# Optimization experiments

Measured on AMD Instinct MI355X. Metric: run time of the kernel, lower is better.

## Reference

```python
import jax, jax.numpy as jnp
import numpy as np

N_HEADS = 16

def setup_inputs() -> dict:
    key = jax.random.key(0)
    ks = jax.random.split(key, 4)
    B, T, C = 4, 2048, 1024
    x = jax.random.normal(ks[0], (B, T, C), dtype=jnp.float32)
    w_qkv = jax.random.normal(ks[1], (C, 3 * C), dtype=jnp.float32) * (1.0 / np.sqrt(C))
    b_qkv = jnp.zeros((3 * C,), dtype=jnp.float32)
    w_proj = jax.random.normal(ks[2], (C, C), dtype=jnp.float32) * (1.0 / np.sqrt(C))
    b_proj = jnp.zeros((C,), dtype=jnp.float32)
    return {"x": x, "w_qkv": w_qkv, "b_qkv": b_qkv, "w_proj": w_proj, "b_proj": b_proj}

def reference(x, w_qkv, b_qkv, w_proj, b_proj):
    B, T, C = x.shape
    H = N_HEADS
    d = C // H
    qkv = x @ w_qkv + b_qkv                       # [B,T,3C]
    q, k, v = jnp.split(qkv, 3, axis=-1)
    # [B,T,C] -> [B,H,T,d]
    q = q.reshape(B, T, H, d).transpose(0, 2, 1, 3)
    k = k.reshape(B, T, H, d).transpose(0, 2, 1, 3)
    v = v.reshape(B, T, H, d).transpose(0, 2, 1, 3)
    scale = 1.0 / np.sqrt(d).astype(np.float32)
    logits = jnp.einsum('bhqd,bhkd->bhqk', q, k) * scale  # [B,H,T,T]
    causal = jnp.tril(jnp.ones((T, T), dtype=bool))
    logits = jnp.where(causal, logits, jnp.finfo(logits.dtype).min)
    attn = jax.nn.softmax(logits, axis=-1)
    out = jnp.einsum('bhqk,bhkd->bhqd', attn, v)          # [B,H,T,d]
    out = out.transpose(0, 2, 1, 3).reshape(B, T, C)
    return out @ w_proj + b_proj
```

## Files before the change

### kernel.cpp

```cpp
#include <hip/hip_runtime.h>
#include <hip/hip_bf16.h>


typedef unsigned short u16;
typedef __bf16 bf16_t;
typedef bf16_t bf16x8 __attribute__((ext_vector_type(8)));
typedef float f32x4 __attribute__((ext_vector_type(4)));
typedef u16 u16x8 __attribute__((ext_vector_type(8)));
typedef const __attribute__((address_space(1))) void* as1cv;
typedef __attribute__((address_space(3))) void* as3v;

#define BB 4
#define TT 2048
#define CC 1024
#define HH 16
#define DD 64

static __device__ __forceinline__ u16 f2bf(float f) {
  union { float f; unsigned int u; } x; x.f = f;
  unsigned int u = x.u;
  u += 0x7fff + ((u >> 16) & 1);
  return (u16)(u >> 16);
}

static __device__ __forceinline__ unsigned int pack2(float lo, float hi) {
  return __builtin_amdgcn_perm(__float_as_uint(hi), __float_as_uint(lo),
                               0x07060302u);
}

__global__ __launch_bounds__(256) void cast_f32_bf16(
    const float* __restrict__ in, u16* __restrict__ out) {
  int i = (blockIdx.x * 256 + threadIdx.x) * 4;
  float4 v = *(const float4*)(in + i);
  ushort4 o;
  o.x = f2bf(v.x); o.y = f2bf(v.y); o.z = f2bf(v.z); o.w = f2bf(v.w);
  *(ushort4*)(out + i) = o;
}

__global__ __launch_bounds__(256) void transpose_cast(
    const float* __restrict__ in, u16* __restrict__ out, int K, int N) {
  __shared__ float tile[32][33];
  int n0 = blockIdx.x * 32, k0 = blockIdx.y * 32;
  int tx = threadIdx.x & 31, ty = threadIdx.x >> 5;
#pragma unroll
  for (int i = 0; i < 32; i += 8)
    tile[ty + i][tx] = in[(size_t)(k0 + ty + i) * N + n0 + tx];
  __syncthreads();
#pragma unroll
  for (int i = 0; i < 32; i += 8)
    out[(size_t)(n0 + ty + i) * K + k0 + tx] = f2bf(tile[tx][ty + i]);
}

__global__ __launch_bounds__(256) void gemm_bt(
    const u16* __restrict__ A, const u16* __restrict__ Bt,
    const float* __restrict__ bias,
    int M, int N, int K, int mode,
    u16* __restrict__ qb, u16* __restrict__ kb, u16* __restrict__ vt,
    float* __restrict__ outf) {
  __shared__ u16 As[128][64];
  __shared__ u16 Bs[128][64];
  const int tid = threadIdx.x;
  const int lane = tid & 63, wave = tid >> 6;
  const int quad = lane >> 4, l16 = lane & 15;
  const int wy = wave >> 1, wx = wave & 1;
  const int m0 = blockIdx.x * 128, n0 = blockIdx.y * 128;
  const int srow = lane >> 3, sblk = (lane & 7) ^ (lane >> 3);
  const int rsw = l16 & 7;

  f32x4 acc[4][4] = {};

  for (int k0 = 0; k0 < K; k0 += 64) {
#pragma unroll
    for (int i = 0; i < 4; i++) {
      int lr = wave * 32 + i * 8;
      int row = lr + srow;
      __builtin_amdgcn_global_load_lds(
          (as1cv)(A + (size_t)(m0 + row) * K + k0 + sblk * 8),
          (as3v)(&As[lr][0]), 16, 0, 0);
      __builtin_amdgcn_global_load_lds(
          (as1cv)(Bt + (size_t)(n0 + row) * K + k0 + sblk * 8),
          (as3v)(&Bs[lr][0]), 16, 0, 0);
    }
    __syncthreads();
#pragma unroll
    for (int ks = 0; ks < 2; ks++) {
      const int pcol = ((ks * 4 + quad) ^ rsw) * 8;
      bf16x8 af[4], bfr[4];
#pragma unroll
      for (int i = 0; i < 4; i++)
        af[i] = *(const bf16x8*)&As[wy * 64 + i * 16 + l16][pcol];
#pragma unroll
      for (int j = 0; j < 4; j++)
        bfr[j] = *(const bf16x8*)&Bs[wx * 64 + j * 16 + l16][pcol];
#pragma unroll
      for (int i = 0; i < 4; i++)
#pragma unroll
        for (int j = 0; j < 4; j++)
          acc[i][j] = __builtin_amdgcn_mfma_f32_16x16x32_bf16(af[i], bfr[j], acc[i][j], 0, 0, 0);
    }
    __syncthreads();
  }

  if (mode == 1) {
#pragma unroll
    for (int i = 0; i < 4; i++)
#pragma unroll
      for (int j = 0; j < 4; j++) {
        int nn = n0 + wx * 64 + j * 16 + l16;
        float bv = bias[nn];
#pragma unroll
        for (int r = 0; r < 4; r++) {
          int mm = m0 + wy * 64 + i * 16 + quad * 4 + r;
          outf[(size_t)mm * N + nn] = acc[i][j][r] + bv;
        }
      }
  } else {
    const int b = m0 >> 11;
    const int tb = (m0 & 2047) + wy * 64 + quad * 4;
    if (n0 < 1024) {
#pragma unroll
      for (int j = 0; j < 4; j++) {
        int nn = n0 + wx * 64 + j * 16 + l16;
        int h = nn >> 6, dd = nn & 63;
        float bv = bias[nn];
        u16* base = qb + ((size_t)(b * HH + h) * TT) * DD + dd;
#pragma unroll
        for (int i = 0; i < 4; i++)
#pragma unroll
          for (int r = 0; r < 4; r++)
            base[(size_t)(tb + i * 16 + r) * DD] =
                f2bf((acc[i][j][r] + bv) * 0.1803368801111f);
      }
    } else if (n0 < 2048) {
#pragma unroll
      for (int j = 0; j < 4; j++) {
        int nn = n0 + wx * 64 + j * 16 + l16;
        int rem = nn & 1023, h = rem >> 6, dd = rem & 63;
        float bv = bias[nn];
        u16* base = kb + ((size_t)(b * HH + h) * TT) * DD + dd;
#pragma unroll
        for (int i = 0; i < 4; i++)
#pragma unroll
          for (int r = 0; r < 4; r++)
            base[(size_t)(tb + i * 16 + r) * DD] = f2bf(acc[i][j][r] + bv);
      }
    } else {
#pragma unroll
      for (int j = 0; j < 4; j++) {
        int nn = n0 + wx * 64 + j * 16 + l16;
        int rem = nn & 1023, h = rem >> 6, dd = rem & 63;
        float bv = bias[nn];
        u16* base = vt + ((size_t)(b * HH + h) * DD + dd) * TT;
#pragma unroll
        for (int i = 0; i < 4; i++)
#pragma unroll
          for (int r = 0; r < 4; r++)
            base[tb + i * 16 + r] = f2bf(acc[i][j][r] + bv);
      }
    }
  }
}

__global__ __launch_bounds__(256, 3) void attn_kernel(
    const u16* __restrict__ q_buf, const u16* __restrict__ k_buf,
    const u16* __restrict__ v_t, u16* __restrict__ attn_out) {
  __shared__ __align__(16) u16 Ks[64][64];
  __shared__ __align__(16) u16 Vs[64][64];
  __shared__ __align__(16) u16 Pl[4][16][64];
  const int tid = threadIdx.x;
  const int lane = tid & 63, wave = tid >> 6;
  const int quad = lane >> 4, l16 = lane & 15;
  const int bh = blockIdx.x;
  const int b = bh >> 4, h = bh & 15;
  const int tile = 15 - (int)blockIdx.y;
  const int qt0 = tile * 128;
  const int qw = qt0 + wave * 32;
  const u16* Q = q_buf + (size_t)bh * TT * DD;
  const u16* Kp = k_buf + (size_t)bh * TT * DD;
  const u16* Vt = v_t + (size_t)bh * DD * TT;

  const int srow = lane >> 3;
  const int sblk = (lane & 7) ^ srow;
  const int swz = l16 & 7;

  bf16x8 qf[2][2];
#pragma unroll
  for (int f = 0; f < 2; f++)
#pragma unroll
    for (int h2 = 0; h2 < 2; h2++)
      qf[f][h2] = *(const bf16x8*)(Q + (size_t)(qw + f * 16 + l16) * DD + h2 * 32 + quad * 8);

  f32x4 o[2][4] = {};
  float l_p[2] = {0.f, 0.f};

  const int my_end = qw + 32;
  const int kv_stop = qt0 + 128;
  for (int kv0 = 0; kv0 < kv_stop; kv0 += 64) {
#pragma unroll
    for (int i = 0; i < 2; i++) {
      int r = wave * 16 + i * 8 + srow;
      __builtin_amdgcn_global_load_lds(
          (as1cv)(Kp + (size_t)(kv0 + r) * DD + sblk * 8),
          (as3v)(&Ks[wave * 16 + i * 8][0]), 16, 0, 0);
      __builtin_amdgcn_global_load_lds(
          (as1cv)(Vt + (size_t)r * TT + kv0 + sblk * 8),
          (as3v)(&Vs[wave * 16 + i * 8][0]), 16, 0, 0);
    }
    __syncthreads();

    if (kv0 < my_end) {
      const bool edge = (kv0 + 63 > qw);
      f32x4 s[2][4] = {};
#pragma unroll
      for (int kg = 0; kg < 4; kg++) {
        bf16x8 ka = *(const bf16x8*)&Ks[kg * 16 + l16][(quad ^ swz) * 8];
        bf16x8 kb2 = *(const bf16x8*)&Ks[kg * 16 + l16][((4 + quad) ^ swz) * 8];
#pragma unroll
        for (int f = 0; f < 2; f++) {
          s[f][kg] = __builtin_amdgcn_mfma_f32_16x16x32_bf16(ka, qf[f][0], s[f][kg], 0, 0, 0);
          s[f][kg] = __builtin_amdgcn_mfma_f32_16x16x32_bf16(kb2, qf[f][1], s[f][kg], 0, 0, 0);
        }
      }
#pragma unroll
      for (int f = 0; f < 2; f++) {
        const int qi = qw + f * 16 + l16;
#pragma unroll
        for (int kg = 0; kg < 4; kg++) {
          float v0 = s[f][kg][0], v1 = s[f][kg][1], v2 = s[f][kg][2], v3 = s[f][kg][3];
          if (edge) {
            int kvb = kv0 + kg * 16 + quad * 4;
            v0 = (kvb + 0 <= qi) ? v0 : -1e30f;
            v1 = (kvb + 1 <= qi) ? v1 : -1e30f;
            v2 = (kvb + 2 <= qi) ? v2 : -1e30f;
            v3 = (kvb + 3 <= qi) ? v3 : -1e30f;
          }
          float e0 = __builtin_amdgcn_exp2f(v0);
          float e1 = __builtin_amdgcn_exp2f(v1);
          float e2 = __builtin_amdgcn_exp2f(v2);
          float e3 = __builtin_amdgcn_exp2f(v3);
          l_p[f] += (e0 + e1) + (e2 + e3);
          uint2 pk;
          pk.x = pack2(e0, e1);
          pk.y = pack2(e2, e3);
          *(uint2*)&Pl[wave][l16][((kg * 2 + (quad >> 1)) ^ swz) * 8 + (quad & 1) * 4] = pk;
        }
        __threadfence_block();
#pragma unroll
        for (int c = 0; c < 2; c++) {
          bf16x8 pa = *(const bf16x8*)&Pl[wave][l16][((c * 4 + quad) ^ swz) * 8];
#pragma unroll
          for (int g = 0; g < 4; g++) {
            bf16x8 vr = *(const bf16x8*)&Vs[g * 16 + l16][((c * 4 + quad) ^ swz) * 8];
            o[f][g] = __builtin_amdgcn_mfma_f32_16x16x32_bf16(vr, pa, o[f][g], 0, 0, 0);
          }
        }
      }
    }
    __syncthreads();
  }

#pragma unroll
  for (int f = 0; f < 2; f++) {
    float l = l_p[f];
    l += __shfl_xor(l, 16);
    l += __shfl_xor(l, 32);
    float inv_l = 1.0f / l;
    int trow = qw + f * 16 + l16;
#pragma unroll
    for (int g = 0; g < 4; g++) {
      ushort4 st;
      st.x = f2bf(o[f][g][0] * inv_l);
      st.y = f2bf(o[f][g][1] * inv_l);
      st.z = f2bf(o[f][g][2] * inv_l);
      st.w = f2bf(o[f][g][3] * inv_l);
      *(ushort4*)(attn_out + ((size_t)(b * TT + trow)) * CC + h * DD + g * 16 + quad * 4) = st;
    }
  }
}

extern "C" void kernel_launch(void* const* d_in, const int* in_sizes, int n_in,
                              void* d_out, int out_size, void* d_ws, size_t ws_size,
                              hipStream_t stream) {
  const float* x = (const float*)d_in[0];
  const float* w_qkv = (const float*)d_in[1];
  const float* b_qkv = (const float*)d_in[2];
  const float* w_proj = (const float*)d_in[3];
  const float* b_proj = (const float*)d_in[4];
  float* out = (float*)d_out;
  char* ws = (char*)d_ws;

  u16* wqkvT = (u16*)(ws);
  u16* wprojT = (u16*)(ws + 6291456);
  u16* qb = (u16*)(ws + 8388608);
  u16* kb = (u16*)(ws + 25165824);
  u16* vt = (u16*)(ws + 41943040);
  u16* ao = (u16*)(ws + 58720256);
  u16* xb = ao;

  cast_f32_bf16<<<dim3(8192), 256, 0, stream>>>(x, xb);
  transpose_cast<<<dim3(96, 32), 256, 0, stream>>>(w_qkv, wqkvT, 1024, 3072);
  transpose_cast<<<dim3(32, 32), 256, 0, stream>>>(w_proj, wprojT, 1024, 1024);
  gemm_bt<<<dim3(64, 24), 256, 0, stream>>>(xb, wqkvT, b_qkv, 8192, 3072, 1024, 0,
                                            qb, kb, vt, nullptr);
  attn_kernel<<<dim3(64, 16), 256, 0, stream>>>(qb, kb, vt, ao);
  gemm_bt<<<dim3(64, 8), 256, 0, stream>>>(ao, wprojT, b_proj, 8192, 1024, 1024, 1,
                                           nullptr, nullptr, nullptr, out);
}
```

Before: 243.4 us.

## Load two KV tiles per barrier and hoist V fragments into registers

The attention loop now stages 128 keys per iteration into two LDS buffers, which halves the number of barrier pairs per query tile. The V fragments are read from LDS once per 64-key block and reused for both query fragments instead of being reloaded per fragment. Launch bounds rise to 4 blocks per CU. The trade-off is more LDS per block (about 40KB) and more registers for the V fragments, which may conflict with the higher occupancy target and cause spills.

```diff
diff --git a/kernel.cpp b/kernel.cpp
--- a/kernel.cpp
+++ b/kernel.cpp
@@ -161,11 +161,11 @@
   }
 }
 
-__global__ __launch_bounds__(256, 3) void attn_kernel(
+__global__ __launch_bounds__(256, 4) void attn_kernel(
     const u16* __restrict__ q_buf, const u16* __restrict__ k_buf,
     const u16* __restrict__ v_t, u16* __restrict__ attn_out) {
-  __shared__ __align__(16) u16 Ks[64][64];
-  __shared__ __align__(16) u16 Vs[64][64];
+  __shared__ __align__(16) u16 Ks[2][64][64];
+  __shared__ __align__(16) u16 Vs[2][64][64];
   __shared__ __align__(16) u16 Pl[4][16][64];
   const int tid = threadIdx.x;
   const int lane = tid & 63, wave = tid >> 6;
@@ -195,63 +195,73 @@
 
   const int my_end = qw + 32;
   const int kv_stop = qt0 + 128;
-  for (int kv0 = 0; kv0 < kv_stop; kv0 += 64) {
-#pragma unroll
-    for (int i = 0; i < 2; i++) {
-      int r = wave * 16 + i * 8 + srow;
-      __builtin_amdgcn_global_load_lds(
-          (as1cv)(Kp + (size_t)(kv0 + r) * DD + sblk * 8),
-          (as3v)(&Ks[wave * 16 + i * 8][0]), 16, 0, 0);
-      __builtin_amdgcn_global_load_lds(
-          (as1cv)(Vt + (size_t)r * TT + kv0 + sblk * 8),
-          (as3v)(&Vs[wave * 16 + i * 8][0]), 16, 0, 0);
-    }
+  for (int kv0 = 0; kv0 < kv_stop; kv0 += 128) {
+#pragma unroll
+    for (int hh = 0; hh < 2; hh++)
+#pragma unroll
+      for (int i = 0; i < 2; i++) {
+        int r = wave * 16 + i * 8 + srow;
+        __builtin_amdgcn_global_load_lds(
+            (as1cv)(Kp + (size_t)(kv0 + hh * 64 + r) * DD + sblk * 8),
+            (as3v)(&Ks[hh][wave * 16 + i * 8][0]), 16, 0, 0);
+        __builtin_amdgcn_global_load_lds(
+            (as1cv)(Vt + (size_t)r * TT + kv0 + hh * 64 + sblk * 8),
+            (as3v)(&Vs[hh][wave * 16 + i * 8][0]), 16, 0, 0);
+      }
     __syncthreads();
 
-    if (kv0 < my_end) {
-      const bool edge = (kv0 + 63 > qw);
-      f32x4 s[2][4] = {};
-#pragma unroll
-      for (int kg = 0; kg < 4; kg++) {
-        bf16x8 ka = *(const bf16x8*)&Ks[kg * 16 + l16][(quad ^ swz) * 8];
-        bf16x8 kb2 = *(const bf16x8*)&Ks[kg * 16 + l16][((4 + quad) ^ swz) * 8];
+#pragma unroll
+    for (int hh = 0; hh < 2; hh++) {
+      const int kb0 = kv0 + hh * 64;
+      if (kb0 < my_end) {
+        const bool edge = (kb0 + 63 > qw);
+        f32x4 s[2][4] = {};
+#pragma unroll
+        for (int kg = 0; kg < 4; kg++) {
+          bf16x8 ka = *(const bf16x8*)&Ks[hh][kg * 16 + l16][(quad ^ swz) * 8];
+          bf16x8 kb2 = *(const bf16x8*)&Ks[hh][kg * 16 + l16][((4 + quad) ^ swz) * 8];
+#pragma unroll
+          for (int f = 0; f < 2; f++) {
+            s[f][kg] = __builtin_amdgcn_mfma_f32_16x16x32_bf16(ka, qf[f][0], s[f][kg], 0, 0, 0);
+            s[f][kg] = __builtin_amdgcn_mfma_f32_16x16x32_bf16(kb2, qf[f][1], s[f][kg], 0, 0, 0);
+          }
+        }
+        bf16x8 vf[4][2];
+#pragma unroll
+        for (int g = 0; g < 4; g++)
+#pragma unroll
+          for (int c = 0; c < 2; c++)
+            vf[g][c] = *(const bf16x8*)&Vs[hh][g * 16 + l16][((c * 4 + quad) ^ swz) * 8];
 #pragma unroll
         for (int f = 0; f < 2; f++) {
-          s[f][kg] = __builtin_amdgcn_mfma_f32_16x16x32_bf16(ka, qf[f][0], s[f][kg], 0, 0, 0);
-          s[f][kg] = __builtin_amdgcn_mfma_f32_16x16x32_bf16(kb2, qf[f][1], s[f][kg], 0, 0, 0);
-        }
-      }
-#pragma unroll
-      for (int f = 0; f < 2; f++) {
-        const int qi = qw + f * 16 + l16;
-#pragma unroll
-        for (int kg = 0; kg < 4; kg++) {
-          float v0 = s[f][kg][0], v1 = s[f][kg][1], v2 = s[f][kg][2], v3 = s[f][kg][3];
-          if (edge) {
-            int kvb = kv0 + kg * 16 + quad * 4;
-            v0 = (kvb + 0 <= qi) ? v0 : -1e30f;
-            v1 = (kvb + 1 <= qi) ? v1 : -1e30f;
-            v2 = (kvb + 2 <= qi) ? v2 : -1e30f;
-            v3 = (kvb + 3 <= qi) ? v3 : -1e30f;
+          const int qi = qw + f * 16 + l16;
+#pragma unroll
+          for (int kg = 0; kg < 4; kg++) {
+            float v0 = s[f][kg][0], v1 = s[f][kg][1], v2 = s[f][kg][2], v3 = s[f][kg][3];
+            if (edge) {
+              int kvb = kb0 + kg * 16 + quad * 4;
+              v0 = (kvb + 0 <= qi) ? v0 : -1e30f;
+              v1 = (kvb + 1 <= qi) ? v1 : -1e30f;
+              v2 = (kvb + 2 <= qi) ? v2 : -1e30f;
+              v3 = (kvb + 3 <= qi) ? v3 : -1e30f;
+            }
+            float e0 = __builtin_amdgcn_exp2f(v0);
+            float e1 = __builtin_amdgcn_exp2f(v1);
+            float e2 = __builtin_amdgcn_exp2f(v2);
+            float e3 = __builtin_amdgcn_exp2f(v3);
+            l_p[f] += (e0 + e1) + (e2 + e3);
+            uint2 pk;
+            pk.x = pack2(e0, e1);
+            pk.y = pack2(e2, e3);
+            *(uint2*)&Pl[wave][l16][((kg * 2 + (quad >> 1)) ^ swz) * 8 + (quad & 1) * 4] = pk;
           }
-          float e0 = __builtin_amdgcn_exp2f(v0);
-          float e1 = __builtin_amdgcn_exp2f(v1);
-          float e2 = __builtin_amdgcn_exp2f(v2);
-          float e3 = __builtin_amdgcn_exp2f(v3);
-          l_p[f] += (e0 + e1) + (e2 + e3);
-          uint2 pk;
-          pk.x = pack2(e0, e1);
-          pk.y = pack2(e2, e3);
-          *(uint2*)&Pl[wave][l16][((kg * 2 + (quad >> 1)) ^ swz) * 8 + (quad & 1) * 4] = pk;
-        }
-        __threadfence_block();
-#pragma unroll
-        for (int c = 0; c < 2; c++) {
-          bf16x8 pa = *(const bf16x8*)&Pl[wave][l16][((c * 4 + quad) ^ swz) * 8];
-#pragma unroll
-          for (int g = 0; g < 4; g++) {
-            bf16x8 vr = *(const bf16x8*)&Vs[g * 16 + l16][((c * 4 + quad) ^ swz) * 8];
-            o[f][g] = __builtin_amdgcn_mfma_f32_16x16x32_bf16(vr, pa, o[f][g], 0, 0, 0);
+          __threadfence_block();
+#pragma unroll
+          for (int c = 0; c < 2; c++) {
+            bf16x8 pa = *(const bf16x8*)&Pl[wave][l16][((c * 4 + quad) ^ swz) * 8];
+#pragma unroll
+            for (int g = 0; g < 4; g++)
+              o[f][g] = __builtin_amdgcn_mfma_f32_16x16x32_bf16(vf[g][c], pa, o[f][g], 0, 0, 0);
           }
         }
       }
```

Measured after the change: 530.5 us. 118% more time.
